# Kernel tuning notes

Hardware: AMD Instinct MI355X
Metric: run time of the kernel (lower is better)

Reference implementation:

```python
import jax, jax.numpy as jnp
import numpy as np

N_NODES = 100000
N_EDGES = 1600000
HID = 128


def setup_inputs() -> dict:
    key = jax.random.key(0)
    ks = jax.random.split(key, 12)
    s = lambda fan_in: 1.0 / np.sqrt(fan_in)
    return {
        "x": jax.random.normal(ks[0], (N_NODES, HID), jnp.float32),
        "edge_index": jax.random.randint(ks[1], (2, N_EDGES), 0, N_NODES, jnp.int64),
        "edge_attr": jax.random.uniform(ks[2], (N_EDGES,), jnp.float32),
        "W_enc": jax.random.normal(ks[3], (HID, HID), jnp.float32) * s(HID),
        "b_enc": jax.random.normal(ks[4], (HID,), jnp.float32) * s(HID),
        "W_msg": jax.random.normal(ks[5], (HID + 1, HID), jnp.float32) * s(HID + 1),
        "b_msg": jax.random.normal(ks[6], (HID,), jnp.float32) * s(HID + 1),
        "W_upd": jax.random.normal(ks[7], (2 * HID, HID), jnp.float32) * s(2 * HID),
        "b_upd": jax.random.normal(ks[8], (HID,), jnp.float32) * s(2 * HID),
        "W_dec": jax.random.normal(ks[9], (HID, 1), jnp.float32) * s(HID),
        "b_dec": jax.random.normal(ks[10], (1,), jnp.float32) * s(HID),
    }


def reference(x, edge_index, edge_attr, W_enc, b_enc, W_msg, b_msg,
              W_upd, b_upd, W_dec, b_dec):
    n = x.shape[0]
    # encoder + relu
    h = jax.nn.relu(x @ W_enc + b_enc)                       # [N, H]
    src, dst = edge_index[0], edge_index[1]
    # message: gather x_j, concat scalar edge_attr, linear
    m = jnp.concatenate([h[src], edge_attr[:, None]], axis=-1) @ W_msg + b_msg  # [E, H]
    # scatter-min aggregate per destination node (nodes w/o in-edges -> 0, PyG convention)
    agg = jax.ops.segment_min(m, dst, num_segments=n)        # [N, H]
    agg = jnp.where(jnp.isinf(agg), jnp.zeros((), m.dtype), agg)
    # update: concat + linear
    u = jnp.concatenate([h, agg], axis=-1) @ W_upd + b_upd   # [N, H]
    # decoder + sigmoid
    return jax.nn.sigmoid(u @ W_dec + b_dec)                 # [N, 1]
```

## Files before the change

kernel.cpp:

```cpp
#include <hip/hip_runtime.h>

#define NN 100000
#define NE 1600000
#define HID 128
#define NBUCK 1563
#define CAP 1280
#define STP 130
#define SENT 3.0e38f
#define CH 4096
#define ENCB 391

typedef float f32x4 __attribute__((ext_vector_type(4)));
typedef __bf16 bf16x8 __attribute__((ext_vector_type(8)));
typedef unsigned short u16x8 __attribute__((ext_vector_type(8)));

static __device__ __forceinline__ unsigned short f2bf(float f) {
  union { float f; unsigned u; } v; v.f = f;
  unsigned u = v.u;
  return (unsigned short)((u + 0x7FFFu + ((u >> 16) & 1u)) >> 16);
}

static __device__ __forceinline__ f32x4 mfma_bf16(u16x8 a, u16x8 b, f32x4 c) {
  return __builtin_amdgcn_mfma_f32_16x16x32_bf16(
      __builtin_bit_cast(bf16x8, a), __builtin_bit_cast(bf16x8, b), c, 0, 0, 0);
}

static __device__ __forceinline__ int gidx(const int* __restrict__ ei, int is64, long long pos) {
  return is64 ? ei[pos * 2] : ei[pos];
}
static __device__ __forceinline__ int detect64(const int* __restrict__ ei, int tid) {
  unsigned long long bl = __ballot(ei[2 * (tid & 63) + 1] == 0);
  return (bl == ~0ull) ? 1 : 0;
}

__global__ __launch_bounds__(512) void k_prepw(const float* __restrict__ Wenc,
    const float* __restrict__ Wmsg, const float* __restrict__ Wupd,
    const float* __restrict__ Wdec, unsigned short* __restrict__ Wb,
    float* __restrict__ vprep, int* __restrict__ gcursor) {
  int b = blockIdx.x;
  int t = threadIdx.x;
  if (b == 96) {
    if (t < 128) {
      const float* row = Wupd + (size_t)(128 + t) * 128;
      float s = 0.f;
#pragma unroll 8
      for (int j = 0; j < 128; ++j) s = fmaf(row[j], Wdec[j], s);
      vprep[t] = s;
    }
    for (int i = t; i < NBUCK; i += 512) gcursor[i] = i * CAP;
    return;
  }
  int i = b * 512 + t;
  int m = i >> 14, idx = i & 16383;
  const float* src = (m == 0) ? Wenc : ((m == 1) ? Wmsg : Wupd);
  int k = idx >> 7, j = idx & 127;
  Wb[m * 17408 + j * 136 + k] = f2bf(src[idx]);
}

__global__ __launch_bounds__(512, 4) void k_work(const float* __restrict__ x,
    const float* __restrict__ benc, const float* __restrict__ bupd,
    const float* __restrict__ Wdec, const unsigned short* __restrict__ Wb,
    const int* __restrict__ ei, const float* __restrict__ ea,
    int* __restrict__ gcursor, unsigned long long* __restrict__ csr,
    unsigned* __restrict__ mNp, float* __restrict__ hdec) {
  __shared__ __align__(16) unsigned short Wt[17408];
  __shared__ unsigned short bounce[8][16 * 136];
  __shared__ unsigned cnt[NBUCK];
  __shared__ float bshE[128];
  __shared__ float bshU[128];
  __shared__ float wdsh[128];
  int tid = threadIdx.x;
  int eb = blockIdx.x;

  for (int i = tid; i < NBUCK; i += 512) cnt[i] = 0;
  if (tid < 128) { bshE[tid] = benc[tid]; bshU[tid] = bupd[tid]; wdsh[tid] = Wdec[tid]; }

  int wave = tid >> 6, lane = tid & 63;
  int l15 = lane & 15, lg = lane >> 4;
  f32x4 zero = {0.f, 0.f, 0.f, 0.f};
  u16x8 haG[2][4];

  for (int i = tid; i < 2176; i += 512)
    ((uint4*)Wt)[i] = ((const uint4*)Wb)[i];
  __syncthreads();
#pragma unroll
  for (int g = 0; g < 2; ++g) {
    int rowBase = eb * 256 + g * 128 + wave * 16;
    int nodeA = rowBase + l15; if (nodeA > NN - 1) nodeA = NN - 1;
    u16x8 af[4];
#pragma unroll
    for (int kt = 0; kt < 4; ++kt) {
      const float* px = x + (long long)nodeA * HID + kt * 32 + lg * 8;
      f32x4 a0 = *(const f32x4*)px;
      f32x4 a1 = *(const f32x4*)(px + 4);
      u16x8 t;
      t[0] = f2bf(a0[0]); t[1] = f2bf(a0[1]); t[2] = f2bf(a0[2]); t[3] = f2bf(a0[3]);
      t[4] = f2bf(a1[0]); t[5] = f2bf(a1[1]); t[6] = f2bf(a1[2]); t[7] = f2bf(a1[3]);
      af[kt] = t;
    }
    f32x4 acc[8];
#pragma unroll
    for (int nt = 0; nt < 8; ++nt) acc[nt] = zero;
#pragma unroll
    for (int kt = 0; kt < 4; ++kt)
#pragma unroll
      for (int nt = 0; nt < 8; ++nt) {
        u16x8 bfv = *(const u16x8*)&Wt[(nt * 16 + l15) * 136 + kt * 32 + lg * 8];
        acc[nt] = mfma_bf16(af[kt], bfv, acc[nt]);
      }
#pragma unroll
    for (int nt = 0; nt < 8; ++nt) {
      int j = nt * 16 + l15;
      float bj = bshE[j];
#pragma unroll
      for (int r = 0; r < 4; ++r) {
        float v = acc[nt][r] + bj;
        v = v > 0.f ? v : 0.f;
        bounce[wave][(lg * 4 + r) * 136 + j] = f2bf(v);
      }
    }
    asm volatile("s_waitcnt lgkmcnt(0)" ::: "memory");
    __builtin_amdgcn_sched_barrier(0);
#pragma unroll
    for (int kt = 0; kt < 4; ++kt)
      haG[g][kt] = *(const u16x8*)&bounce[wave][l15 * 136 + kt * 32 + lg * 8];
    asm volatile("s_waitcnt lgkmcnt(0)" ::: "memory");
    __builtin_amdgcn_sched_barrier(0);
  }

  unsigned long long ereg[CH / 512];
  {
    long long base = (long long)eb * CH;
    int n = (int)(((long long)NE - base < CH) ? ((long long)NE - base) : CH);
    if (n < 0) n = 0;
    int is64 = detect64(ei, tid);
#pragma unroll
    for (int k = 0; k < CH / 512; ++k) {
      int i = k * 512 + tid;
      if (i < n) {
        int s = gidx(ei, is64, base + i);
        int d = gidx(ei, is64, (long long)NE + base + i);
        unsigned eab = f2bf(ea[base + i]);
        unsigned bkt = (unsigned)(d >> 6);
        unsigned lo = (unsigned)(s << 6) | ((unsigned)(d & 63) << 23);
        unsigned hi = (eab << 16) | bkt;
        ereg[k] = (unsigned long long)lo | ((unsigned long long)hi << 32);
        atomicAdd(&cnt[bkt], 1u);
      } else ereg[k] = 0xFFFFFFFFFFFFFFFFull;
    }
  }
  __syncthreads();

  for (int i = tid; i < 2176; i += 512)
    ((uint4*)Wt)[i] = ((const uint4*)Wb)[2176 + i];
  __syncthreads();
#pragma unroll
  for (int g = 0; g < 2; ++g) {
    int rowBase = eb * 256 + g * 128 + wave * 16;
    f32x4 acc2[8];
#pragma unroll
    for (int nt = 0; nt < 8; ++nt) acc2[nt] = zero;
#pragma unroll
    for (int kt = 0; kt < 4; ++kt)
#pragma unroll
      for (int nt = 0; nt < 8; ++nt) {
        u16x8 bfv = *(const u16x8*)&Wt[(nt * 16 + l15) * 136 + kt * 32 + lg * 8];
        acc2[nt] = mfma_bf16(haG[g][kt], bfv, acc2[nt]);
      }
#pragma unroll
    for (int nt = 0; nt < 8; ++nt) {
      int j = nt * 16 + l15;
#pragma unroll
      for (int r = 0; r < 4; ++r)
        bounce[wave][(lg * 4 + r) * 136 + j] = f2bf(acc2[nt][r]);
    }
    asm volatile("s_waitcnt lgkmcnt(0)" ::: "memory");
    __builtin_amdgcn_sched_barrier(0);
#pragma unroll 4
    for (int row = 0; row < 16; ++row) {
      int node = rowBase + row;
      if (node < NN) {
        unsigned lo = bounce[wave][row * 136 + lane];
        unsigned hi = bounce[wave][row * 136 + 64 + lane];
        mNp[(size_t)node * 64 + lane] = lo | (hi << 16);
      }
    }
    asm volatile("s_waitcnt lgkmcnt(0)" ::: "memory");
    __builtin_amdgcn_sched_barrier(0);
  }
  __syncthreads();

  for (int i = tid; i < 2176; i += 512)
    ((uint4*)Wt)[i] = ((const uint4*)Wb)[4352 + i];
  __syncthreads();
#pragma unroll
  for (int g = 0; g < 2; ++g) {
    int rowBase = eb * 256 + g * 128 + wave * 16;
    f32x4 acc3[8];
#pragma unroll
    for (int nt = 0; nt < 8; ++nt) acc3[nt] = zero;
#pragma unroll
    for (int kt = 0; kt < 4; ++kt)
#pragma unroll
      for (int nt = 0; nt < 8; ++nt) {
        u16x8 bfv = *(const u16x8*)&Wt[(nt * 16 + l15) * 136 + kt * 32 + lg * 8];
        acc3[nt] = mfma_bf16(haG[g][kt], bfv, acc3[nt]);
      }
    float hs0 = 0.f, hs1 = 0.f, hs2 = 0.f, hs3 = 0.f;
#pragma unroll
    for (int nt = 0; nt < 8; ++nt) {
      int j = nt * 16 + l15;
      float bu = bshU[j], wv = wdsh[j];
      hs0 += (acc3[nt][0] + bu) * wv;
      hs1 += (acc3[nt][1] + bu) * wv;
      hs2 += (acc3[nt][2] + bu) * wv;
      hs3 += (acc3[nt][3] + bu) * wv;
    }
#pragma unroll
    for (int m = 1; m < 16; m <<= 1) {
      hs0 += __shfl_xor(hs0, m);
      hs1 += __shfl_xor(hs1, m);
      hs2 += __shfl_xor(hs2, m);
      hs3 += __shfl_xor(hs3, m);
    }
    if (l15 == 0) {
      int n0 = rowBase + lg * 4;
      if (n0 + 3 < NN) {
        float4 st4; st4.x = hs0; st4.y = hs1; st4.z = hs2; st4.w = hs3;
        *(float4*)&hdec[n0] = st4;
      } else {
        if (n0 + 0 < NN) hdec[n0 + 0] = hs0;
        if (n0 + 1 < NN) hdec[n0 + 1] = hs1;
        if (n0 + 2 < NN) hdec[n0 + 2] = hs2;
        if (n0 + 3 < NN) hdec[n0 + 3] = hs3;
      }
    }
  }
  __syncthreads();

  {
    unsigned* gbase = (unsigned*)&bounce[0][0];
    for (int b = tid; b < NBUCK; b += 512) {
      unsigned c = cnt[b];
      gbase[b] = c ? (unsigned)atomicAdd(&gcursor[b], (int)c) : 0u;
    }
    __syncthreads();
    for (int i = tid; i < NBUCK; i += 512) cnt[i] = 0;
    __syncthreads();
#pragma unroll
    for (int k = 0; k < CH / 512; ++k) {
      unsigned long long e = ereg[k];
      unsigned bkt = (unsigned)(e >> 32) & 0xFFFFu;
      if (bkt != 0xFFFFu) {
        unsigned lp = atomicAdd(&cnt[bkt], 1u);
        csr[gbase[bkt] + lp] = e;
      }
    }
  }
}

__global__ __launch_bounds__(512, 8) void k_msg(const unsigned* __restrict__ mNp,
    const float* __restrict__ Wmsg, const int* __restrict__ gcursor,
    const unsigned long long* __restrict__ csr, const float* __restrict__ bmsg,
    const float* __restrict__ vprep, const float* __restrict__ hdec,
    const float* __restrict__ bdec, float* __restrict__ out) {
  __shared__ float stf[64 * STP];
  int tid = threadIdx.x;
  int b = blockIdx.x;
  for (int i = tid; i < 64 * STP; i += 512) stf[i] = SENT;
  __syncthreads();

  int lane = tid & 63;
  int wv = tid >> 6;
  int off = b * CAP, end = gcursor[b];
  int cntE = end - off;
  int per = (cntE + 7) >> 3;
  int i0 = off + wv * per;
  int i1 = i0 + per; if (i1 > end) i1 = end;
  int iu = __builtin_amdgcn_readfirstlane(i0);
  int ie = __builtin_amdgcn_readfirstlane(i1);
  float wl0 = Wmsg[128 * 128 + lane];
  float wl1 = Wmsg[128 * 128 + 64 + lane];

#define EDGE_DO(PK, VV) do { \
    int loc_ = (int)(((unsigned)(PK) >> 23) & 0x3Fu); \
    float ea_ = __uint_as_float((unsigned)((PK) >> 32) & 0xFFFF0000u); \
    float a0_ = fmaf(ea_, wl0, __uint_as_float((VV) << 16)); \
    float a1_ = fmaf(ea_, wl1, __uint_as_float((VV) & 0xFFFF0000u)); \
    atomicMin(&stf[loc_ * STP + lane], a0_); \
    atomicMin(&stf[loc_ * STP + 64 + lane], a1_); \
  } while (0)

  int i = iu;
  for (; i + 16 <= ie; i += 16) {
    unsigned long long pk[16];
#pragma unroll
    for (int j = 0; j < 16; ++j) pk[j] = csr[i + j];
    unsigned v[16];
#pragma unroll
    for (int j = 0; j < 16; ++j)
      v[j] = mNp[((unsigned)pk[j] & 0x7FFFFFu) + lane];
#pragma unroll
    for (int j = 0; j < 16; ++j) EDGE_DO(pk[j], v[j]);
  }
  for (; i + 4 <= ie; i += 4) {
    unsigned long long pk[4];
#pragma unroll
    for (int j = 0; j < 4; ++j) pk[j] = csr[i + j];
    unsigned v[4];
#pragma unroll
    for (int j = 0; j < 4; ++j)
      v[j] = mNp[((unsigned)pk[j] & 0x7FFFFFu) + lane];
#pragma unroll
    for (int j = 0; j < 4; ++j) EDGE_DO(pk[j], v[j]);
  }
  for (; i < ie; ++i) {
    unsigned long long pk = csr[i];
    unsigned v = mNp[((unsigned)pk & 0x7FFFFFu) + lane];
    EDGE_DO(pk, v);
  }
#undef EDGE_DO
  __syncthreads();

  float vl0 = vprep[lane], vl1 = vprep[64 + lane];
  float bm0 = bmsg[lane], bm1 = bmsg[64 + lane];
  float bd = *bdec;
#pragma unroll
  for (int q = 0; q < 8; ++q) {
    int loc = (wv << 3) + q;
    float s0 = stf[loc * STP + lane];
    float s1 = stf[loc * STP + 64 + lane];
    float ps = ((s0 < 1.0e30f) ? (s0 + bm0) * vl0 : 0.f)
             + ((s1 < 1.0e30f) ? (s1 + bm1) * vl1 : 0.f);
#pragma unroll
    for (int m = 1; m < 64; m <<= 1) ps += __shfl_xor(ps, m);
    if (lane == 0) {
      int node = (b << 6) + loc;
      if (node < NN)
        out[node] = 1.f / (1.f + expf(-(ps + hdec[node] + bd)));
    }
  }
}

extern "C" void kernel_launch(void* const* d_in, const int* in_sizes, int n_in,
                              void* d_out, int out_size, void* d_ws, size_t ws_size,
                              hipStream_t stream) {
  const float* x    = (const float*)d_in[0];
  const int*   ei   = (const int*)d_in[1];
  const float* ea   = (const float*)d_in[2];
  const float* Wenc = (const float*)d_in[3];
  const float* benc = (const float*)d_in[4];
  const float* Wmsg = (const float*)d_in[5];
  const float* bmsg = (const float*)d_in[6];
  const float* Wupd = (const float*)d_in[7];
  const float* bupd = (const float*)d_in[8];
  const float* Wdec = (const float*)d_in[9];
  const float* bdec = (const float*)d_in[10];
  float* out = (float*)d_out;

  char* w = (char*)d_ws;
  auto alloc = [&](size_t bytes) { char* p = w; w += (bytes + 255) & ~(size_t)255; return p; };
  unsigned* mNp        = (unsigned*)alloc((size_t)NN * 64 * 4);
  unsigned long long* csr = (unsigned long long*)alloc((size_t)NBUCK * CAP * 8);
  unsigned short* Wb = (unsigned short*)alloc(3 * 17408 * 2);
  float* hdec   = (float*)alloc((size_t)NN * 4);
  float* vprep  = (float*)alloc(128 * 4);
  int* gcursor  = (int*)alloc((size_t)NBUCK * 4);

  k_prepw<<<97, 512, 0, stream>>>(Wenc, Wmsg, Wupd, Wdec, Wb, vprep, gcursor);
  k_work<<<ENCB, 512, 0, stream>>>(x, benc, bupd, Wdec, Wb, ei, ea,
                                   gcursor, csr, mNp, hdec);
  k_msg<<<NBUCK, 512, 0, stream>>>(mNp, Wmsg, gcursor, csr, bmsg, vprep, hdec, bdec, out);
}
```

Measured before the change: 114.1 us.

## Interleave message rows so each wavefront gathers two edges per 64-bit load

The producer now writes each node's packed bf16 message row with an interleaved column order. In the message kernel, each half-wave gathers a different edge's 256-byte row through 64-bit loads, so one wave handles two edges per load instruction, each lane doing four atomic mins. This halves the number of gather instructions and loop iterations per edge but doubles the LDS atomics per lane per step. The tail loop now processes edges in pairs and duplicates the last edge when the count is odd, which is harmless for min.

```diff
diff --git a/kernel.cpp b/kernel.cpp
--- a/kernel.cpp
+++ b/kernel.cpp
@@ -182,7 +182,7 @@
       if (node < NN) {
         unsigned lo = bounce[wave][row * 136 + lane];
         unsigned hi = bounce[wave][row * 136 + 64 + lane];
-        mNp[(size_t)node * 64 + lane] = lo | (hi << 16);
+        mNp[(size_t)node * 64 + 2 * (lane & 31) + (lane >> 5)] = lo | (hi << 16);
       }
     }
     asm volatile("s_waitcnt lgkmcnt(0)" ::: "memory");
@@ -259,7 +259,7 @@
   }
 }
 
-__global__ __launch_bounds__(512, 8) void k_msg(const unsigned* __restrict__ mNp,
+__global__ __launch_bounds__(512, 8) void k_msg(const unsigned long long* __restrict__ mNp64,
     const float* __restrict__ Wmsg, const int* __restrict__ gcursor,
     const unsigned long long* __restrict__ csr, const float* __restrict__ bmsg,
     const float* __restrict__ vprep, const float* __restrict__ hdec,
@@ -271,6 +271,8 @@
   __syncthreads();
 
   int lane = tid & 63;
+  int lp = lane & 31;
+  int hiHalf = lane >> 5;
   int wv = tid >> 6;
   int off = b * CAP, end = gcursor[b];
   int cntE = end - off;
@@ -279,47 +281,51 @@
   int i1 = i0 + per; if (i1 > end) i1 = end;
   int iu = __builtin_amdgcn_readfirstlane(i0);
   int ie = __builtin_amdgcn_readfirstlane(i1);
-  float wl0 = Wmsg[128 * 128 + lane];
-  float wl1 = Wmsg[128 * 128 + 64 + lane];
-
-#define EDGE_DO(PK, VV) do { \
-    int loc_ = (int)(((unsigned)(PK) >> 23) & 0x3Fu); \
-    float ea_ = __uint_as_float((unsigned)((PK) >> 32) & 0xFFFF0000u); \
-    float a0_ = fmaf(ea_, wl0, __uint_as_float((VV) << 16)); \
-    float a1_ = fmaf(ea_, wl1, __uint_as_float((VV) & 0xFFFF0000u)); \
-    atomicMin(&stf[loc_ * STP + lane], a0_); \
-    atomicMin(&stf[loc_ * STP + 64 + lane], a1_); \
+  float wlA = Wmsg[128 * 128 + lp];
+  float wlB = Wmsg[128 * 128 + 32 + lp];
+  float wlC = Wmsg[128 * 128 + 64 + lp];
+  float wlD = Wmsg[128 * 128 + 96 + lp];
+
+#define PROCP(EA, EB, V) do { \
+    unsigned long long e_ = hiHalf ? (EB) : (EA); \
+    float ea_ = __uint_as_float((unsigned)(e_ >> 32) & 0xFFFF0000u); \
+    int loc_ = (int)(((unsigned)e_ >> 23) & 63u); \
+    unsigned lo32_ = (unsigned)(V), hi32_ = (unsigned)((V) >> 32); \
+    float a0_ = fmaf(ea_, wlA, __uint_as_float(lo32_ << 16)); \
+    float a1_ = fmaf(ea_, wlC, __uint_as_float(lo32_ & 0xFFFF0000u)); \
+    float a2_ = fmaf(ea_, wlB, __uint_as_float(hi32_ << 16)); \
+    float a3_ = fmaf(ea_, wlD, __uint_as_float(hi32_ & 0xFFFF0000u)); \
+    atomicMin(&stf[loc_ * STP + lp], a0_); \
+    atomicMin(&stf[loc_ * STP + 32 + lp], a2_); \
+    atomicMin(&stf[loc_ * STP + 64 + lp], a1_); \
+    atomicMin(&stf[loc_ * STP + 96 + lp], a3_); \
   } while (0)
+
+#define ROW64(E) ((((unsigned)(E) & 0x7FFFFFu) >> 1) + (unsigned)lp)
 
   int i = iu;
   for (; i + 16 <= ie; i += 16) {
     unsigned long long pk[16];
 #pragma unroll
     for (int j = 0; j < 16; ++j) pk[j] = csr[i + j];
-    unsigned v[16];
-#pragma unroll
-    for (int j = 0; j < 16; ++j)
-      v[j] = mNp[((unsigned)pk[j] & 0x7FFFFFu) + lane];
-#pragma unroll
-    for (int j = 0; j < 16; ++j) EDGE_DO(pk[j], v[j]);
-  }
-  for (; i + 4 <= ie; i += 4) {
-    unsigned long long pk[4];
-#pragma unroll
-    for (int j = 0; j < 4; ++j) pk[j] = csr[i + j];
-    unsigned v[4];
-#pragma unroll
-    for (int j = 0; j < 4; ++j)
-      v[j] = mNp[((unsigned)pk[j] & 0x7FFFFFu) + lane];
-#pragma unroll
-    for (int j = 0; j < 4; ++j) EDGE_DO(pk[j], v[j]);
-  }
-  for (; i < ie; ++i) {
-    unsigned long long pk = csr[i];
-    unsigned v = mNp[((unsigned)pk & 0x7FFFFFu) + lane];
-    EDGE_DO(pk, v);
-  }
-#undef EDGE_DO
+    unsigned long long v[8];
+#pragma unroll
+    for (int p = 0; p < 8; ++p) {
+      unsigned long long sel = hiHalf ? pk[2 * p + 1] : pk[2 * p];
+      v[p] = mNp64[ROW64(sel)];
+    }
+#pragma unroll
+    for (int p = 0; p < 8; ++p) PROCP(pk[2 * p], pk[2 * p + 1], v[p]);
+  }
+  for (; i < ie; i += 2) {
+    unsigned long long pkA = csr[i];
+    unsigned long long pkB = (i + 1 < ie) ? csr[i + 1] : pkA;
+    unsigned long long sel = hiHalf ? pkB : pkA;
+    unsigned long long v = mNp64[ROW64(sel)];
+    PROCP(pkA, pkB, v);
+  }
+#undef PROCP
+#undef ROW64
   __syncthreads();
 
   float vl0 = vprep[lane], vl1 = vprep[64 + lane];
@@ -370,5 +376,6 @@
   k_prepw<<<97, 512, 0, stream>>>(Wenc, Wmsg, Wupd, Wdec, Wb, vprep, gcursor);
   k_work<<<ENCB, 512, 0, stream>>>(x, benc, bupd, Wdec, Wb, ei, ea,
                                    gcursor, csr, mNp, hdec);
-  k_msg<<<NBUCK, 512, 0, stream>>>(mNp, Wmsg, gcursor, csr, bmsg, vprep, hdec, bdec, out);
-}
+  k_msg<<<NBUCK, 512, 0, stream>>>((const unsigned long long*)mNp, Wmsg, gcursor, csr,
+                                   bmsg, vprep, hdec, bdec, out);
+}
```

After: 287.8 us. 2.52x slower.
